# Kernel tuning notes

Hardware: AMD Instinct MI355X
Metric: run time of the kernel (lower is better)

The kernel has to match this reference:

```python
import jax, jax.numpy as jnp
import numpy as np

N = 100000   # nodes
E = 1200000  # edges
D = 64       # emb_dim
XIN = 18     # x_dim + node_dim
XD = 16      # x_dim (output)
ED = 1       # edge_dim
L = 4        # num message-passing layers
G = 8        # graphs in batch (for global_mean_pool)


def setup_inputs() -> dict:
    key = jax.random.key(0)
    ks = iter(jax.random.split(key, 64))
    def nrm(shape, s=0.05):
        return jax.random.normal(next(ks), shape, dtype=jnp.float32) * s
    inp = {}
    inp["x"] = jax.random.normal(next(ks), (N, XIN), dtype=jnp.float32)
    inp["edge_attr"] = jax.random.normal(next(ks), (E, ED), dtype=jnp.float32)
    inp["W_in"] = nrm((XIN, D)); inp["b_in"] = jnp.zeros((D,), jnp.float32)
    # per-layer stacked params (leading dim L)
    inp["msg_W1"] = nrm((L, 2 * D + ED, D)); inp["msg_b1"] = jnp.zeros((L, D), jnp.float32)
    inp["msg_g1"] = jnp.ones((L, D), jnp.float32); inp["msg_be1"] = jnp.zeros((L, D), jnp.float32)
    inp["msg_W2"] = nrm((L, D, D)); inp["msg_b2"] = jnp.zeros((L, D), jnp.float32)
    inp["msg_g2"] = jnp.ones((L, D), jnp.float32); inp["msg_be2"] = jnp.zeros((L, D), jnp.float32)
    inp["upd_W1"] = nrm((L, 2 * D, D)); inp["upd_b1"] = jnp.zeros((L, D), jnp.float32)
    inp["upd_g1"] = jnp.ones((L, D), jnp.float32); inp["upd_be1"] = jnp.zeros((L, D), jnp.float32)
    inp["upd_W2"] = nrm((L, D, D)); inp["upd_b2"] = jnp.zeros((L, D), jnp.float32)
    inp["upd_g2"] = jnp.ones((L, D), jnp.float32); inp["upd_be2"] = jnp.zeros((L, D), jnp.float32)
    inp["reward_W"] = nrm((D, D)); inp["reward_b"] = jnp.zeros((D,), jnp.float32)
    inp["rout_W"] = nrm((D, 1)); inp["rout_b"] = jnp.zeros((1,), jnp.float32)
    inp["pred_W"] = nrm((D, D)); inp["pred_b"] = jnp.zeros((D,), jnp.float32)
    inp["pout_W"] = nrm((D, XD)); inp["pout_b"] = jnp.zeros((XD,), jnp.float32)
    inp["edge_index"] = jax.random.randint(next(ks), (2, E), 0, N)
    inp["batch"] = jnp.sort(jax.random.randint(next(ks), (N,), 0, G))
    return inp


def _bn(x, g, b, eps=1e-5):
    # BatchNorm1d in training mode: batch mean + biased variance
    m = jnp.mean(x, axis=0)
    v = jnp.mean((x - m) ** 2, axis=0)
    return (x - m) * jax.lax.rsqrt(v + eps) * g + b


def _mlp(x, W1, b1, g1, be1, W2, b2, g2, be2):
    h = jax.nn.relu(_bn(x @ W1 + b1, g1, be1))
    return jax.nn.relu(_bn(h @ W2 + b2, g2, be2))


def _forward(x, edge_attr, W_in, b_in,
             msg_W1, msg_b1, msg_g1, msg_be1, msg_W2, msg_b2, msg_g2, msg_be2,
             upd_W1, upd_b1, upd_g1, upd_be1, upd_W2, upd_b2, upd_g2, upd_be2,
             reward_W, reward_b, rout_W, rout_b, pred_W, pred_b, pout_W, pout_b,
             edge_index, batch):
    src = edge_index[0]  # j (source)
    dst = edge_index[1]  # i (target); PyG default flow source_to_target
    n = x.shape[0]
    h = x @ W_in + b_in
    for l in range(L):
        # message: gather + concat + MLP(psi)
        m = jnp.concatenate([h[dst], h[src], edge_attr], axis=-1)  # (E, 2D+ED)
        m = _mlp(m, msg_W1[l], msg_b1[l], msg_g1[l], msg_be1[l],
                 msg_W2[l], msg_b2[l], msg_g2[l], msg_be2[l])
        # aggregate: scatter-add to target nodes
        agg = jax.ops.segment_sum(m, dst, num_segments=n)  # (N, D)
        # update: concat + MLP(phi); residual add from outer network
        u = jnp.concatenate([h, agg], axis=-1)
        h = h + _mlp(u, upd_W1[l], upd_b1[l], upd_g1[l], upd_be1[l],
                     upd_W2[l], upd_b2[l], upd_g2[l], upd_be2[l])
    # reward head (computed in the original forward but not returned)
    h_reward = h @ reward_W + reward_b
    cnt = jax.ops.segment_sum(jnp.ones((n,), h.dtype), batch, num_segments=G)
    h_graph = jax.ops.segment_sum(h_reward, batch, num_segments=G) / jnp.maximum(cnt, 1.0)[:, None]
    _out_reward = h_graph @ rout_W + rout_b  # unused, matches original return
    # prediction head
    x_out = jax.nn.relu(h @ pred_W + pred_b) @ pout_W + pout_b  # (N, XD)
    return x_out


def reference(x, edge_attr, W_in, b_in,
              msg_W1, msg_b1, msg_g1, msg_be1, msg_W2, msg_b2, msg_g2, msg_be2,
              upd_W1, upd_b1, upd_g1, upd_be1, upd_W2, upd_b2, upd_g2, upd_be2,
              reward_W, reward_b, rout_W, rout_b, pred_W, pred_b, pout_W, pout_b,
              edge_index, batch):
    return _forward(x, edge_attr, W_in, b_in,
                    msg_W1, msg_b1, msg_g1, msg_be1, msg_W2, msg_b2, msg_g2, msg_be2,
                    upd_W1, upd_b1, upd_g1, upd_be1, upd_W2, upd_b2, upd_g2, upd_be2,
                    reward_W, reward_b, rout_W, rout_b, pred_W, pred_b, pout_W, pout_b,
                    edge_index, batch)
```

## Files before the change

### kernel.cpp

```cpp
#include <hip/hip_runtime.h>
#include <hip/hip_fp16.h>

typedef unsigned short u16;
typedef unsigned int u32;
typedef __attribute__((ext_vector_type(8))) unsigned short us8;
typedef __attribute__((ext_vector_type(8))) _Float16 f16x8;
typedef __attribute__((ext_vector_type(4))) float f32x4;

#define EPS 1e-5f

__device__ __forceinline__ float h2f(u16 h){ __half v; *(u16*)&v = h; return __half2float(v); }
__device__ __forceinline__ u16 f2h(float f){ __half v = __float2half(f); return *(u16*)&v; }
__device__ __forceinline__ u32 pkh(float a, float b){ return (u32)f2h(a) | ((u32)f2h(b) << 16); }

__global__ __launch_bounds__(256) void k_in(const float* __restrict__ x,
    const float* __restrict__ Win, const float* __restrict__ bin,
    float* __restrict__ h, int N){
  __shared__ float Ws[18][64];
  __shared__ float xs[64][20];
  int tid = threadIdx.x;
  for (int i = tid; i < 18*64; i += 256) Ws[i>>6][i&63] = Win[i];
  int row0 = blockIdx.x * 64;
  for (int i = tid; i < 64*18; i += 256){
    int r = i/18, k = i - r*18;
    int row = row0 + r;
    xs[r][k] = (row < N) ? x[(size_t)row*18 + k] : 0.f;
  }
  __syncthreads();
  int rq = tid >> 4, dq = tid & 15;
  float4 b4 = *(const float4*)(bin + dq*4);
  float acc[4][4];
  #pragma unroll
  for (int j=0;j<4;j++){ acc[j][0]=b4.x; acc[j][1]=b4.y; acc[j][2]=b4.z; acc[j][3]=b4.w; }
  for (int k=0;k<18;k++){
    float4 wv = *(const float4*)&Ws[k][dq*4];
    #pragma unroll
    for (int j=0;j<4;j++){
      float v = xs[rq*4+j][k];
      acc[j][0]+=v*wv.x; acc[j][1]+=v*wv.y; acc[j][2]+=v*wv.z; acc[j][3]+=v*wv.w;
    }
  }
  #pragma unroll
  for (int j=0;j<4;j++){
    int row = row0 + rq*4 + j;
    if (row < N)
      *(float4*)(h + (size_t)row*64 + dq*4) = make_float4(acc[j][0],acc[j][1],acc[j][2],acc[j][3]);
  }
}

__global__ __launch_bounds__(256) void k_pq(const float* __restrict__ h,
    const float* __restrict__ A, const float* __restrict__ B,
    u16* __restrict__ P, u16* __restrict__ Q, int N){
  __shared__ float hs[64][68];
  __shared__ float As[64][64];
  __shared__ float Bs[64][64];
  int tid = threadIdx.x;
  for (int i = tid; i < 4096; i += 256){ As[i>>6][i&63] = A[i]; Bs[i>>6][i&63] = B[i]; }
  int row0 = blockIdx.x*64;
  for (int i = tid; i < 4096; i += 256){
    int r = i>>6, k = i&63; int row = row0+r;
    hs[r][k] = (row<N)? h[(size_t)row*64+k] : 0.f;
  }
  __syncthreads();
  int rq = tid>>4, dq = tid&15;
  float ap[4][4]={}, aq[4][4]={};
  for (int k=0;k<64;k+=4){
    float4 hv[4];
    #pragma unroll
    for (int j=0;j<4;j++) hv[j] = *(const float4*)&hs[rq*4+j][k];
    #pragma unroll
    for (int kk=0;kk<4;kk++){
      float4 av = *(const float4*)&As[k+kk][dq*4];
      float4 bv = *(const float4*)&Bs[k+kk][dq*4];
      #pragma unroll
      for (int j=0;j<4;j++){
        float v = ((const float*)&hv[j])[kk];
        ap[j][0]+=v*av.x; ap[j][1]+=v*av.y; ap[j][2]+=v*av.z; ap[j][3]+=v*av.w;
        aq[j][0]+=v*bv.x; aq[j][1]+=v*bv.y; aq[j][2]+=v*bv.z; aq[j][3]+=v*bv.w;
      }
    }
  }
  #pragma unroll
  for (int j=0;j<4;j++){
    int row = row0 + rq*4 + j;
    if (row<N){
      ushort4 pk, qk;
      pk.x=f2h(ap[j][0]); pk.y=f2h(ap[j][1]); pk.z=f2h(ap[j][2]); pk.w=f2h(ap[j][3]);
      qk.x=f2h(aq[j][0]); qk.y=f2h(aq[j][1]); qk.z=f2h(aq[j][2]); qk.w=f2h(aq[j][3]);
      *(ushort4*)(P+(size_t)row*64+dq*4) = pk;
      *(ushort4*)(Q+(size_t)row*64+dq*4) = qk;
    }
  }
}

__global__ __launch_bounds__(256) void k_hist(const int* __restrict__ ei, int* __restrict__ cnt, int E){
  int e = blockIdx.x*256 + threadIdx.x;
  if (e < E) atomicAdd(&cnt[ei[E+e]], 1);
}

__global__ __launch_bounds__(256) void k_scan_a(const int* __restrict__ cnt, int* __restrict__ rp,
    int* __restrict__ bsum, int N){
  __shared__ int sm[256];
  int tid = threadIdx.x;
  int i0 = blockIdx.x*1024 + tid*4;
  int v0 = (i0+0<N)? cnt[i0+0]:0;
  int v1 = (i0+1<N)? cnt[i0+1]:0;
  int v2 = (i0+2<N)? cnt[i0+2]:0;
  int v3 = (i0+3<N)? cnt[i0+3]:0;
  int s = v0+v1+v2+v3;
  sm[tid] = s; __syncthreads();
  for (int ofs=1; ofs<256; ofs<<=1){
    int v = sm[tid];
    if (tid >= ofs) v += sm[tid-ofs];
    __syncthreads(); sm[tid] = v; __syncthreads();
  }
  int base = sm[tid] - s;
  int a0 = base+v0, a1 = a0+v1, a2 = a1+v2, a3 = a2+v3;
  if (i0+0<N) rp[i0+0]=a0;
  if (i0+1<N) rp[i0+1]=a1;
  if (i0+2<N) rp[i0+2]=a2;
  if (i0+3<N) rp[i0+3]=a3;
  if (tid==255) bsum[blockIdx.x] = sm[255];
}

__global__ void k_scan_b(int* __restrict__ bsum, int NB){
  if (threadIdx.x==0){
    int run = 0;
    for (int b=0;b<NB;b++){ int t = bsum[b]; bsum[b] = run; run += t; }
  }
}

__global__ __launch_bounds__(256) void k_scan_c(const int* __restrict__ cnt, int* __restrict__ rp,
    int* __restrict__ wr, const int* __restrict__ bsum, int N, int E){
  int tid = threadIdx.x;
  int i0 = blockIdx.x*1024 + tid*4;
  int off = bsum[blockIdx.x];
  #pragma unroll
  for (int j=0;j<4;j++){
    int i = i0+j;
    if (i<N){ int ex = off + rp[i] - cnt[i]; rp[i] = ex; wr[i] = ex; }
  }
  if (blockIdx.x==0 && tid==0) rp[N] = E;
}

__global__ __launch_bounds__(256) void k_perm(const int* __restrict__ ei, const float* __restrict__ ea,
    int* __restrict__ wr, int2* __restrict__ seS, int E){
  int e = blockIdx.x*256 + threadIdx.x;
  if (e < E){
    int dn = ei[E+e];
    int pos = atomicAdd(&wr[dn], 1);
    seS[pos] = make_int2(ei[e], __float_as_int(ea[e]));
  }
}

__global__ __launch_bounds__(256) void k_t1s(const u16* __restrict__ P, const u16* __restrict__ Q,
    const int2* __restrict__ seS, const int* __restrict__ rp,
    const float* __restrict__ c1, const float* __restrict__ b1,
    u16* __restrict__ t, float* __restrict__ stats, int N){
  int tid = threadIdx.x;
  int lane = tid & 63, w = tid >> 6;
  int sub = lane >> 5;
  int dl = (lane & 31) * 2;
  float cv0 = c1[dl], cv1 = c1[dl+1];
  float bv0 = b1[dl], bv1 = b1[dl+1];
  float s0 = 0.f, s1 = 0.f, qs0 = 0.f, qs1 = 0.f;
  for (int n = blockIdx.x*4 + w; n < N; n += gridDim.x*4){
    int a = rp[n], b = rp[n+1];
    u32 pp = *(const u32*)(P + (size_t)n*64 + dl);
    float p0 = h2f((u16)(pp & 0xffffu)) + bv0;
    float p1 = h2f((u16)(pp >> 16)) + bv1;
    int p = a + sub;
    for (; p + 2 < b; p += 4){
      int2 seA = seS[p];
      int2 seB = seS[p+2];
      u32 qA = *(const u32*)(Q + (size_t)seA.x*64 + dl);
      u32 qB = *(const u32*)(Q + (size_t)seB.x*64 + dl);
      float eaA = __int_as_float(seA.y), eaB = __int_as_float(seB.y);
      float tA0 = p0 + h2f((u16)(qA & 0xffffu)) + eaA*cv0;
      float tA1 = p1 + h2f((u16)(qA >> 16)) + eaA*cv1;
      float tB0 = p0 + h2f((u16)(qB & 0xffffu)) + eaB*cv0;
      float tB1 = p1 + h2f((u16)(qB >> 16)) + eaB*cv1;
      *(u32*)(t + (size_t)p*64 + dl) = (u32)f2h(tA0) | ((u32)f2h(tA1) << 16);
      *(u32*)(t + (size_t)(p+2)*64 + dl) = (u32)f2h(tB0) | ((u32)f2h(tB1) << 16);
      s0 += tA0 + tB0; s1 += tA1 + tB1;
      qs0 += tA0*tA0 + tB0*tB0; qs1 += tA1*tA1 + tB1*tB1;
    }
    for (; p < b; p += 2){
      int2 se = seS[p];
      u32 qq = *(const u32*)(Q + (size_t)se.x*64 + dl);
      float ea = __int_as_float(se.y);
      float t0 = p0 + h2f((u16)(qq & 0xffffu)) + ea*cv0;
      float t1 = p1 + h2f((u16)(qq >> 16)) + ea*cv1;
      *(u32*)(t + (size_t)p*64 + dl) = (u32)f2h(t0) | ((u32)f2h(t1) << 16);
      s0 += t0; s1 += t1; qs0 += t0*t0; qs1 += t1*t1;
    }
  }
  __shared__ float sS[8][64], qS[8][64];
  int idx = w*2 + sub;
  sS[idx][dl] = s0; sS[idx][dl+1] = s1;
  qS[idx][dl] = qs0; qS[idx][dl+1] = qs1;
  __syncthreads();
  if (tid < 64){
    float ts = 0.f, tq = 0.f;
    #pragma unroll
    for (int r=0;r<8;r++){ ts += sS[r][tid]; tq += qS[r][tid]; }
    atomicAdd(&stats[tid], ts);
    atomicAdd(&stats[64+tid], tq);
  }
}

__global__ __launch_bounds__(256) void k_m2s(u16* __restrict__ t,
    const float* __restrict__ g1, const float* __restrict__ be1, const float* __restrict__ stats1,
    const float* __restrict__ W2, const float* __restrict__ b2,
    float* __restrict__ stats2, int E, float invE){
  __shared__ _Float16 yL[128][72];
  __shared__ _Float16 wL[64][72];
  __shared__ float scS[64], shS[64], b2S[64];
  int tid = threadIdx.x;
  if (tid < 64){
    float m = stats1[tid]*invE;
    float v = stats1[64+tid]*invE - m*m;
    float sc = g1[tid]*rsqrtf(v + EPS);
    scS[tid] = sc; shS[tid] = be1[tid] - m*sc;
    b2S[tid] = b2[tid];
  }
  for (int i = tid; i < 4096; i += 256){
    int k = i >> 6, n = i & 63;
    wL[n][k] = (_Float16)W2[i];
  }
  __syncthreads();
  int lane = tid & 63, wv = tid >> 6;
  int arow = lane & 15;
  int kgrp = lane >> 4;
  int srow = tid >> 1, sc0 = (tid & 1)*32;
  float ssum[4] = {}, ssq[4] = {};
  int ntiles = (E + 127) >> 7;
  for (int tile = blockIdx.x; tile < ntiles; tile += gridDim.x){
    int e0 = tile << 7;
    {
      int p = e0 + srow;
      if (p < E){
        const u16* src = t + (size_t)p*64 + sc0;
        #pragma unroll
        for (int c=0;c<4;c++){
          f16x8 a = *(const f16x8*)(src + c*8);
          f16x8 v;
          #pragma unroll
          for (int j=0;j<8;j++){
            int dd = sc0 + c*8 + j;
            v[j] = (_Float16)fmaxf((float)a[j]*scS[dd] + shS[dd], 0.f);
          }
          *(f16x8*)&yL[srow][sc0 + c*8] = v;
        }
      } else {
        f16x8 z;
        #pragma unroll
        for (int j=0;j<8;j++) z[j] = (_Float16)0.f;
        #pragma unroll
        for (int c=0;c<4;c++) *(f16x8*)&yL[srow][sc0 + c*8] = z;
      }
    }
    __syncthreads();
    f32x4 acc[2][4];
    #pragma unroll
    for (int mf=0; mf<2; mf++){
      int row = 32*wv + 16*mf + arow;
      f16x8 a0 = *(const f16x8*)&yL[row][8*kgrp];
      f16x8 a1 = *(const f16x8*)&yL[row][32 + 8*kgrp];
      #pragma unroll
      for (int c=0;c<4;c++){
        f16x8 b0 = *(const f16x8*)&wL[16*c + arow][8*kgrp];
        f16x8 b1 = *(const f16x8*)&wL[16*c + arow][32 + 8*kgrp];
        f32x4 d = {0.f,0.f,0.f,0.f};
        d = __builtin_amdgcn_mfma_f32_16x16x32_f16(a0, b0, d, 0, 0, 0);
        d = __builtin_amdgcn_mfma_f32_16x16x32_f16(a1, b1, d, 0, 0, 0);
        acc[mf][c] = d;
      }
    }
    __syncthreads();
    #pragma unroll
    for (int mf=0; mf<2; mf++){
      #pragma unroll
      for (int c=0;c<4;c++){
        int col = 16*c + arow;
        float bb = b2S[col];
        #pragma unroll
        for (int r=0;r<4;r++){
          int e = e0 + 32*wv + 16*mf + 4*kgrp + r;
          if (e < E){
            float v = acc[mf][c][r] + bb;
            t[(size_t)e*64 + col] = f2h(v);
            ssum[c] += v; ssq[c] += v*v;
          }
        }
      }
    }
  }
  __syncthreads();
  float* red = (float*)yL;
  #pragma unroll
  for (int c=0;c<4;c++) red[c*256 + tid] = ssum[c];
  __syncthreads();
  if (tid < 64){
    int cc = tid >> 4;
    float s = 0.f;
    for (int g=0; g<16; g++) s += red[cc*256 + g*16 + (tid & 15)];
    atomicAdd(&stats2[tid], s);
  }
  __syncthreads();
  #pragma unroll
  for (int c=0;c<4;c++) red[c*256 + tid] = ssq[c];
  __syncthreads();
  if (tid < 64){
    int cc = tid >> 4;
    float s = 0.f;
    for (int g=0; g<16; g++) s += red[cc*256 + g*16 + (tid & 15)];
    atomicAdd(&stats2[64+tid], s);
  }
}

__global__ __launch_bounds__(256) void k_agg(const u16* __restrict__ t2, const int* __restrict__ rp,
    const float* __restrict__ g2, const float* __restrict__ be2, const float* __restrict__ stats2,
    float* __restrict__ agg, int N, float invE){
  __shared__ float scS[64], shS[64];
  int tid = threadIdx.x;
  if (tid < 64){
    float m = stats2[tid]*invE;
    float v = stats2[64+tid]*invE - m*m;
    float sc = g2[tid]*rsqrtf(v+EPS);
    scS[tid] = sc; shS[tid] = be2[tid] - m*sc;
  }
  __syncthreads();
  int lane = tid & 63, w = tid >> 6;
  int sub = lane >> 5;
  int dl = (lane & 31) * 2;
  float sc0 = scS[dl], sc1 = scS[dl+1], sh0 = shS[dl], sh1 = shS[dl+1];
  for (int n = blockIdx.x*4 + w; n < N; n += gridDim.x*4){
    int a = rp[n], b = rp[n+1];
    float a0 = 0.f, a1 = 0.f;
    int p = a + sub;
    for (; p + 2 < b; p += 4){
      u32 vA = *(const u32*)(t2 + (size_t)p*64 + dl);
      u32 vB = *(const u32*)(t2 + (size_t)(p+2)*64 + dl);
      a0 += fmaxf(h2f((u16)(vA & 0xffffu))*sc0 + sh0, 0.f)
          + fmaxf(h2f((u16)(vB & 0xffffu))*sc0 + sh0, 0.f);
      a1 += fmaxf(h2f((u16)(vA >> 16))*sc1 + sh1, 0.f)
          + fmaxf(h2f((u16)(vB >> 16))*sc1 + sh1, 0.f);
    }
    for (; p < b; p += 2){
      u32 vA = *(const u32*)(t2 + (size_t)p*64 + dl);
      a0 += fmaxf(h2f((u16)(vA & 0xffffu))*sc0 + sh0, 0.f);
      a1 += fmaxf(h2f((u16)(vA >> 16))*sc1 + sh1, 0.f);
    }
    a0 += __shfl_xor(a0, 32);
    a1 += __shfl_xor(a1, 32);
    if (sub == 0)
      *(float2*)(agg + (size_t)n*64 + dl) = make_float2(a0, a1);
  }
}

__global__ __launch_bounds__(256) void k_s1(const u16* __restrict__ P, const u16* __restrict__ Q,
    const float* __restrict__ ea, const int* __restrict__ ei,
    const float* __restrict__ c1, const float* __restrict__ b1,
    float* __restrict__ stats, int E){
  int tid = threadIdx.x;
  int d = tid & 63, w = tid >> 6;
  float cv = c1[d], bv = b1[d];
  float s = 0.f, sq = 0.f;
  for (int e = blockIdx.x*4 + w; e < E; e += gridDim.x*4){
    int dn = ei[E+e], sn = ei[e];
    float t = h2f(P[(size_t)dn*64+d]) + h2f(Q[(size_t)sn*64+d]) + ea[e]*cv + bv;
    s += t; sq += t*t;
  }
  __shared__ float sS[4][64], qS[4][64];
  sS[w][d] = s; qS[w][d] = sq;
  __syncthreads();
  if (tid < 64){
    float ts = sS[0][tid]+sS[1][tid]+sS[2][tid]+sS[3][tid];
    float tq = qS[0][tid]+qS[1][tid]+qS[2][tid]+qS[3][tid];
    atomicAdd(&stats[tid], ts);
    atomicAdd(&stats[64+tid], tq);
  }
}

__global__ __launch_bounds__(256) void k_m2b(const u16* __restrict__ P, const u16* __restrict__ Q,
    const float* __restrict__ ea, const int* __restrict__ ei,
    const float* __restrict__ c1, const float* __restrict__ b1,
    const float* __restrict__ g1, const float* __restrict__ be1,
    const float* __restrict__ stats1,
    const float* __restrict__ W2, const float* __restrict__ b2,
    float* __restrict__ stats2, int E, float invE){
  __shared__ float ys[64][68];
  __shared__ float Ws[64][64];
  __shared__ float scS[64], c1S[64], bS[64], b2S[64];
  int tid = threadIdx.x;
  if (tid < 64){
    float m = stats1[tid]*invE;
    float v = stats1[64+tid]*invE - m*m;
    float sc = g1[tid]*rsqrtf(v + EPS);
    float sh = be1[tid] - m*sc;
    scS[tid] = sc;
    c1S[tid] = c1[tid]*sc;
    bS[tid]  = b1[tid]*sc + sh;
    b2S[tid] = b2[tid];
  }
  for (int i=tid;i<4096;i+=256) Ws[i>>6][i&63] = W2[i];
  __syncthreads();
  int rq = tid>>4, dq = tid&15;
  float ssum[4]={}, ssq[4]={};
  int ntiles = (E+63)>>6;
  for (int tile = blockIdx.x; tile < ntiles; tile += gridDim.x){
    int e0 = tile<<6;
    for (int i = tid; i < 4096; i += 256){
      int el = i>>6, dd = i&63;
      int e = e0 + el;
      float y = 0.f;
      if (e < E){
        int dn = ei[E+e], sn = ei[e];
        float t = (h2f(P[(size_t)dn*64+dd]) + h2f(Q[(size_t)sn*64+dd]))*scS[dd] + ea[e]*c1S[dd] + bS[dd];
        y = fmaxf(t, 0.f);
      }
      ys[el][dd] = y;
    }
    __syncthreads();
    float acc[4][4];
    float4 b4 = *(const float4*)&b2S[dq*4];
    #pragma unroll
    for (int j=0;j<4;j++){ acc[j][0]=b4.x; acc[j][1]=b4.y; acc[j][2]=b4.z; acc[j][3]=b4.w; }
    for (int k=0;k<64;k+=4){
      float4 hv[4];
      #pragma unroll
      for (int j=0;j<4;j++) hv[j] = *(const float4*)&ys[rq*4+j][k];
      #pragma unroll
      for (int kk=0;kk<4;kk++){
        float4 wv = *(const float4*)&Ws[k+kk][dq*4];
        #pragma unroll
        for (int j=0;j<4;j++){
          float v = ((const float*)&hv[j])[kk];
          acc[j][0]+=v*wv.x; acc[j][1]+=v*wv.y; acc[j][2]+=v*wv.z; acc[j][3]+=v*wv.w;
        }
      }
    }
    #pragma unroll
    for (int j=0;j<4;j++){
      int e = e0 + rq*4 + j;
      if (e < E){
        #pragma unroll
        for (int c=0;c<4;c++){ float v=acc[j][c]; ssum[c]+=v; ssq[c]+=v*v; }
      }
    }
    __syncthreads();
  }
  float* red = &ys[0][0];
  #pragma unroll
  for (int c=0;c<4;c++) red[rq*64 + dq*4 + c] = ssum[c];
  __syncthreads();
  if (tid < 64){
    float t=0.f;
    for (int r=0;r<16;r++) t += red[r*64+tid];
    atomicAdd(&stats2[tid], t);
  }
  __syncthreads();
  #pragma unroll
  for (int c=0;c<4;c++) red[rq*64 + dq*4 + c] = ssq[c];
  __syncthreads();
  if (tid < 64){
    float t=0.f;
    for (int r=0;r<16;r++) t += red[r*64+tid];
    atomicAdd(&stats2[64+tid], t);
  }
}

__global__ __launch_bounds__(256) void k_sc_rec(const u16* __restrict__ P, const u16* __restrict__ Q,
    const float* __restrict__ ea, const int* __restrict__ ei,
    const float* __restrict__ c1, const float* __restrict__ b1,
    const float* __restrict__ g1, const float* __restrict__ be1, const float* __restrict__ stats1,
    const float* __restrict__ W2, const float* __restrict__ b2,
    const float* __restrict__ g2, const float* __restrict__ be2, const float* __restrict__ stats2,
    float* __restrict__ agg, int E, float invE){
  __shared__ float ys[64][68];
  __shared__ float Ws[64][64];
  __shared__ float scS[64], c1S[64], bS[64];
  __shared__ float s2S[64], h2S[64], b2S[64];
  int tid = threadIdx.x;
  if (tid < 64){
    float m = stats1[tid]*invE;
    float v = stats1[64+tid]*invE - m*m;
    float sc = g1[tid]*rsqrtf(v + EPS);
    scS[tid] = sc;
    c1S[tid] = c1[tid]*sc;
    bS[tid]  = b1[tid]*sc + be1[tid] - m*sc;
    float m2 = stats2[tid]*invE;
    float v2 = stats2[64+tid]*invE - m2*m2;
    float sc2 = g2[tid]*rsqrtf(v2+EPS);
    s2S[tid] = sc2; h2S[tid] = be2[tid] - m2*sc2;
    b2S[tid] = b2[tid];
  }
  for (int i=tid;i<4096;i+=256) Ws[i>>6][i&63] = W2[i];
  __syncthreads();
  int rq = tid>>4, dq = tid&15;
  int ntiles = (E+63)>>6;
  for (int tile = blockIdx.x; tile < ntiles; tile += gridDim.x){
    int e0 = tile<<6;
    for (int i = tid; i < 4096; i += 256){
      int el = i>>6, dd = i&63;
      int e = e0 + el;
      float y = 0.f;
      if (e < E){
        int dn = ei[E+e], sn = ei[e];
        float t = (h2f(P[(size_t)dn*64+dd]) + h2f(Q[(size_t)sn*64+dd]))*scS[dd] + ea[e]*c1S[dd] + bS[dd];
        y = fmaxf(t, 0.f);
      }
      ys[el][dd] = y;
    }
    __syncthreads();
    float acc[4][4];
    float4 b4 = *(const float4*)&b2S[dq*4];
    #pragma unroll
    for (int j=0;j<4;j++){ acc[j][0]=b4.x; acc[j][1]=b4.y; acc[j][2]=b4.z; acc[j][3]=b4.w; }
    for (int k=0;k<64;k+=4){
      float4 hv[4];
      #pragma unroll
      for (int j=0;j<4;j++) hv[j] = *(const float4*)&ys[rq*4+j][k];
      #pragma unroll
      for (int kk=0;kk<4;kk++){
        float4 wv = *(const float4*)&Ws[k+kk][dq*4];
        #pragma unroll
        for (int j=0;j<4;j++){
          float v = ((const float*)&hv[j])[kk];
          acc[j][0]+=v*wv.x; acc[j][1]+=v*wv.y; acc[j][2]+=v*wv.z; acc[j][3]+=v*wv.w;
        }
      }
    }
    float4 sc4 = *(const float4*)&s2S[dq*4];
    float4 sh4 = *(const float4*)&h2S[dq*4];
    #pragma unroll
    for (int j=0;j<4;j++){
      int e = e0 + rq*4 + j;
      if (e < E){
        int dn = ei[E+e];
        float y0 = fmaxf(acc[j][0]*sc4.x + sh4.x, 0.f);
        float y1 = fmaxf(acc[j][1]*sc4.y + sh4.y, 0.f);
        float y2 = fmaxf(acc[j][2]*sc4.z + sh4.z, 0.f);
        float y3 = fmaxf(acc[j][3]*sc4.w + sh4.w, 0.f);
        atomicAdd(&agg[(size_t)dn*64 + dq*4    ], y0);
        atomicAdd(&agg[(size_t)dn*64 + dq*4 + 1], y1);
        atomicAdd(&agg[(size_t)dn*64 + dq*4 + 2], y2);
        atomicAdd(&agg[(size_t)dn*64 + dq*4 + 3], y3);
      }
    }
    __syncthreads();
  }
}

__global__ __launch_bounds__(256) void k_up1(const float* __restrict__ h, const float* __restrict__ agg,
    const float* __restrict__ U1, const float* __restrict__ b1u,
    float* __restrict__ tn, float* __restrict__ stats3, int N){
  __shared__ _Float16 yL[64][136];
  __shared__ _Float16 wL[64][136];
  __shared__ float bS[64];
  int tid = threadIdx.x;
  if (tid < 64) bS[tid] = b1u[tid];
  for (int i = tid; i < 8192; i += 256){
    int k = i >> 6, n = i & 63;
    wL[n][k] = (_Float16)U1[i];
  }
  int row0 = blockIdx.x * 64;
  int srow = tid >> 2, sc0 = (tid & 3) * 16;
  {
    int row = row0 + srow;
    if (row < N){
      #pragma unroll
      for (int c=0;c<4;c++){
        float4 v = *(const float4*)(h + (size_t)row*64 + sc0 + 4*c);
        *(u32*)&yL[srow][sc0+4*c]   = pkh(v.x, v.y);
        *(u32*)&yL[srow][sc0+4*c+2] = pkh(v.z, v.w);
      }
      #pragma unroll
      for (int c=0;c<4;c++){
        float4 v = *(const float4*)(agg + (size_t)row*64 + sc0 + 4*c);
        *(u32*)&yL[srow][64+sc0+4*c]   = pkh(v.x, v.y);
        *(u32*)&yL[srow][64+sc0+4*c+2] = pkh(v.z, v.w);
      }
    } else {
      #pragma unroll
      for (int c=0;c<4;c++){
        *(u32*)&yL[srow][sc0+4*c] = 0u; *(u32*)&yL[srow][sc0+4*c+2] = 0u;
        *(u32*)&yL[srow][64+sc0+4*c] = 0u; *(u32*)&yL[srow][64+sc0+4*c+2] = 0u;
      }
    }
  }
  __syncthreads();
  int lane = tid & 63, wv = tid >> 6;
  int arow = lane & 15, kgrp = lane >> 4;
  f16x8 a[4];
  #pragma unroll
  for (int kk=0;kk<4;kk++) a[kk] = *(const f16x8*)&yL[16*wv + arow][32*kk + 8*kgrp];
  float ssum[4]={}, ssq[4]={};
  #pragma unroll
  for (int c=0;c<4;c++){
    f32x4 d = {0.f,0.f,0.f,0.f};
    #pragma unroll
    for (int kk=0;kk<4;kk++){
      f16x8 b = *(const f16x8*)&wL[16*c + arow][32*kk + 8*kgrp];
      d = __builtin_amdgcn_mfma_f32_16x16x32_f16(a[kk], b, d, 0, 0, 0);
    }
    int col = 16*c + arow;
    float bb = bS[col];
    #pragma unroll
    for (int r=0;r<4;r++){
      int row = row0 + 16*wv + 4*kgrp + r;
      if (row < N){
        float v = d[r] + bb;
        tn[(size_t)row*64 + col] = v;
        ssum[c]+=v; ssq[c]+=v*v;
      }
    }
  }
  __syncthreads();
  float* red = (float*)yL;
  #pragma unroll
  for (int c=0;c<4;c++) red[c*256 + tid] = ssum[c];
  __syncthreads();
  if (tid < 64){
    int cc = tid >> 4;
    float s = 0.f;
    for (int g=0; g<16; g++) s += red[cc*256 + g*16 + (tid & 15)];
    atomicAdd(&stats3[tid], s);
  }
  __syncthreads();
  #pragma unroll
  for (int c=0;c<4;c++) red[c*256 + tid] = ssq[c];
  __syncthreads();
  if (tid < 64){
    int cc = tid >> 4;
    float s = 0.f;
    for (int g=0; g<16; g++) s += red[cc*256 + g*16 + (tid & 15)];
    atomicAdd(&stats3[64+tid], s);
  }
}

__global__ __launch_bounds__(256) void k_up2(float* __restrict__ tn,
    const float* __restrict__ g3, const float* __restrict__ be3, const float* __restrict__ stats3,
    const float* __restrict__ U2, const float* __restrict__ b2u,
    float* __restrict__ stats4, int N, float invN){
  __shared__ _Float16 yL[64][72];
  __shared__ _Float16 wL[64][72];
  __shared__ float scS[64], shS[64], bS[64];
  int tid = threadIdx.x;
  if (tid < 64){
    float m = stats3[tid]*invN;
    float v = stats3[64+tid]*invN - m*m;
    float sc = g3[tid]*rsqrtf(v+EPS);
    scS[tid] = sc; shS[tid] = be3[tid] - m*sc; bS[tid] = b2u[tid];
  }
  for (int i = tid; i < 4096; i += 256){
    int k = i >> 6, n = i & 63;
    wL[n][k] = (_Float16)U2[i];
  }
  __syncthreads();
  int row0 = blockIdx.x * 64;
  int srow = tid >> 2, sc0 = (tid & 3) * 16;
  {
    int row = row0 + srow;
    if (row < N){
      #pragma unroll
      for (int c=0;c<4;c++){
        float4 v = *(const float4*)(tn + (size_t)row*64 + sc0 + 4*c);
        int d0 = sc0 + 4*c;
        float y0 = fmaxf(v.x*scS[d0  ] + shS[d0  ], 0.f);
        float y1 = fmaxf(v.y*scS[d0+1] + shS[d0+1], 0.f);
        float y2 = fmaxf(v.z*scS[d0+2] + shS[d0+2], 0.f);
        float y3 = fmaxf(v.w*scS[d0+3] + shS[d0+3], 0.f);
        *(u32*)&yL[srow][d0]   = pkh(y0, y1);
        *(u32*)&yL[srow][d0+2] = pkh(y2, y3);
      }
    } else {
      #pragma unroll
      for (int c=0;c<4;c++){
        *(u32*)&yL[srow][sc0+4*c] = 0u; *(u32*)&yL[srow][sc0+4*c+2] = 0u;
      }
    }
  }
  __syncthreads();
  int lane = tid & 63, wv = tid >> 6;
  int arow = lane & 15, kgrp = lane >> 4;
  f16x8 a0 = *(const f16x8*)&yL[16*wv + arow][8*kgrp];
  f16x8 a1 = *(const f16x8*)&yL[16*wv + arow][32 + 8*kgrp];
  float ssum[4]={}, ssq[4]={};
  #pragma unroll
  for (int c=0;c<4;c++){
    f16x8 b0 = *(const f16x8*)&wL[16*c + arow][8*kgrp];
    f16x8 b1 = *(const f16x8*)&wL[16*c + arow][32 + 8*kgrp];
    f32x4 d = {0.f,0.f,0.f,0.f};
    d = __builtin_amdgcn_mfma_f32_16x16x32_f16(a0, b0, d, 0, 0, 0);
    d = __builtin_amdgcn_mfma_f32_16x16x32_f16(a1, b1, d, 0, 0, 0);
    int col = 16*c + arow;
    float bb = bS[col];
    #pragma unroll
    for (int r=0;r<4;r++){
      int row = row0 + 16*wv + 4*kgrp + r;
      if (row < N){
        float v = d[r] + bb;
        tn[(size_t)row*64 + col] = v;
        ssum[c]+=v; ssq[c]+=v*v;
      }
    }
  }
  __syncthreads();
  float* red = (float*)yL;
  #pragma unroll
  for (int c=0;c<4;c++) red[c*256 + tid] = ssum[c];
  __syncthreads();
  if (tid < 64){
    int cc = tid >> 4;
    float s = 0.f;
    for (int g=0; g<16; g++) s += red[cc*256 + g*16 + (tid & 15)];
    atomicAdd(&stats4[tid], s);
  }
  __syncthreads();
  #pragma unroll
  for (int c=0;c<4;c++) red[c*256 + tid] = ssq[c];
  __syncthreads();
  if (tid < 64){
    int cc = tid >> 4;
    float s = 0.f;
    for (int g=0; g<16; g++) s += red[cc*256 + g*16 + (tid & 15)];
    atomicAdd(&stats4[64+tid], s);
  }
}

__global__ __launch_bounds__(256) void k_res_pq(float* __restrict__ h, const float* __restrict__ tn,
    const float* __restrict__ g4, const float* __restrict__ be4, const float* __restrict__ stats4,
    const float* __restrict__ A, const float* __restrict__ B,
    u16* __restrict__ P, u16* __restrict__ Q, int N, float invN){
  __shared__ _Float16 yL[64][72];
  __shared__ _Float16 wLa[64][72];
  __shared__ _Float16 wLb[64][72];
  __shared__ float scS[64], shS[64];
  int tid = threadIdx.x;
  if (tid < 64){
    float m = stats4[tid]*invN;
    float v = stats4[64+tid]*invN - m*m;
    float sc = g4[tid]*rsqrtf(v+EPS);
    scS[tid] = sc; shS[tid] = be4[tid] - m*sc;
  }
  for (int i = tid; i < 4096; i += 256){
    int k = i >> 6, n = i & 63;
    wLa[n][k] = (_Float16)A[i];
    wLb[n][k] = (_Float16)B[i];
  }
  __syncthreads();
  int row0 = blockIdx.x * 64;
  int srow = tid >> 2, sc0 = (tid & 3) * 16;
  {
    int row = row0 + srow;
    if (row < N){
      #pragma unroll
      for (int c=0;c<4;c++){
        int d0 = sc0 + 4*c;
        float4 hv4 = *(const float4*)(h + (size_t)row*64 + d0);
        float4 tv4 = *(const float4*)(tn + (size_t)row*64 + d0);
        float h0 = hv4.x + fmaxf(tv4.x*scS[d0  ] + shS[d0  ], 0.f);
        float h1 = hv4.y + fmaxf(tv4.y*scS[d0+1] + shS[d0+1], 0.f);
        float h2 = hv4.z + fmaxf(tv4.z*scS[d0+2] + shS[d0+2], 0.f);
        float h3 = hv4.w + fmaxf(tv4.w*scS[d0+3] + shS[d0+3], 0.f);
        *(float4*)(h + (size_t)row*64 + d0) = make_float4(h0,h1,h2,h3);
        *(u32*)&yL[srow][d0]   = pkh(h0, h1);
        *(u32*)&yL[srow][d0+2] = pkh(h2, h3);
      }
    } else {
      #pragma unroll
      for (int c=0;c<4;c++){
        *(u32*)&yL[srow][sc0+4*c] = 0u; *(u32*)&yL[srow][sc0+4*c+2] = 0u;
      }
    }
  }
  __syncthreads();
  int lane = tid & 63, wv = tid >> 6;
  int arow = lane & 15, kgrp = lane >> 4;
  f16x8 y0 = *(const f16x8*)&yL[16*wv + arow][8*kgrp];
  f16x8 y1 = *(const f16x8*)&yL[16*wv + arow][32 + 8*kgrp];
  int node = row0 + 16*wv + arow;
  #pragma unroll
  for (int c=0;c<4;c++){
    f16x8 wa0 = *(const f16x8*)&wLa[16*c + arow][8*kgrp];
    f16x8 wa1 = *(const f16x8*)&wLa[16*c + arow][32 + 8*kgrp];
    f32x4 dp = {0.f,0.f,0.f,0.f};
    dp = __builtin_amdgcn_mfma_f32_16x16x32_f16(wa0, y0, dp, 0, 0, 0);
    dp = __builtin_amdgcn_mfma_f32_16x16x32_f16(wa1, y1, dp, 0, 0, 0);
    f16x8 wb0 = *(const f16x8*)&wLb[16*c + arow][8*kgrp];
    f16x8 wb1 = *(const f16x8*)&wLb[16*c + arow][32 + 8*kgrp];
    f32x4 dq = {0.f,0.f,0.f,0.f};
    dq = __builtin_amdgcn_mfma_f32_16x16x32_f16(wb0, y0, dq, 0, 0, 0);
    dq = __builtin_amdgcn_mfma_f32_16x16x32_f16(wb1, y1, dq, 0, 0, 0);
    if (node < N){
      ushort4 pk4, qk4;
      pk4.x = f2h(dp[0]); pk4.y = f2h(dp[1]); pk4.z = f2h(dp[2]); pk4.w = f2h(dp[3]);
      qk4.x = f2h(dq[0]); qk4.y = f2h(dq[1]); qk4.z = f2h(dq[2]); qk4.w = f2h(dq[3]);
      *(ushort4*)(P + (size_t)node*64 + 16*c + 4*kgrp) = pk4;
      *(ushort4*)(Q + (size_t)node*64 + 16*c + 4*kgrp) = qk4;
    }
  }
}

__global__ __launch_bounds__(256) void k_res_head(const float* __restrict__ h, const float* __restrict__ tn,
    const float* __restrict__ g4, const float* __restrict__ be4, const float* __restrict__ stats4,
    const float* __restrict__ Wp, const float* __restrict__ bp,
    const float* __restrict__ Wo, const float* __restrict__ bo,
    float* __restrict__ out, int N, float invN){
  __shared__ float hs[64][68];
  __shared__ float Wps[64][64];
  __shared__ float ps[64][68];
  __shared__ float Wos[64][16];
  __shared__ float scS[64], shS[64];
  int tid = threadIdx.x;
  if (tid < 64){
    float m = stats4[tid]*invN;
    float v = stats4[64+tid]*invN - m*m;
    float sc = g4[tid]*rsqrtf(v+EPS);
    scS[tid] = sc; shS[tid] = be4[tid] - m*sc;
  }
  for (int i=tid;i<4096;i+=256) Wps[i>>6][i&63] = Wp[i];
  for (int i=tid;i<1024;i+=256) Wos[i>>4][i&15] = Wo[i];
  int row0 = blockIdx.x*64;
  __syncthreads();
  for (int i = tid; i < 4096; i += 256){
    int r = i>>6, k = i&63; int row = row0+r;
    float hv = 0.f;
    if (row<N)
      hv = h[(size_t)row*64+k] + fmaxf(tn[(size_t)row*64+k]*scS[k] + shS[k], 0.f);
    hs[r][k] = hv;
  }
  __syncthreads();
  int rq = tid>>4, dq = tid&15;
  float4 b4 = *(const float4*)(bp + dq*4);
  float acc[4][4];
  #pragma unroll
  for (int j=0;j<4;j++){ acc[j][0]=b4.x; acc[j][1]=b4.y; acc[j][2]=b4.z; acc[j][3]=b4.w; }
  for (int k=0;k<64;k+=4){
    float4 hv[4];
    #pragma unroll
    for (int j=0;j<4;j++) hv[j] = *(const float4*)&hs[rq*4+j][k];
    #pragma unroll
    for (int kk=0;kk<4;kk++){
      float4 wv = *(const float4*)&Wps[k+kk][dq*4];
      #pragma unroll
      for (int j=0;j<4;j++){
        float v = ((const float*)&hv[j])[kk];
        acc[j][0]+=v*wv.x; acc[j][1]+=v*wv.y; acc[j][2]+=v*wv.z; acc[j][3]+=v*wv.w;
      }
    }
  }
  #pragma unroll
  for (int j=0;j<4;j++){
    *(float4*)&ps[rq*4+j][dq*4] = make_float4(fmaxf(acc[j][0],0.f), fmaxf(acc[j][1],0.f),
                                              fmaxf(acc[j][2],0.f), fmaxf(acc[j][3],0.f));
  }
  __syncthreads();
  int f = tid & 15;
  float bof = bo[f];
  float acc2[4] = {bof, bof, bof, bof};
  for (int k=0;k<64;k++){
    float wv = Wos[k][f];
    #pragma unroll
    for (int j=0;j<4;j++) acc2[j] += ps[rq*4+j][k]*wv;
  }
  #pragma unroll
  for (int j=0;j<4;j++){
    int row = row0 + rq*4 + j;
    if (row<N) out[(size_t)row*16 + f] = acc2[j];
  }
}

extern "C" void kernel_launch(void* const* d_in, const int* in_sizes, int n_in,
                              void* d_out, int out_size, void* d_ws, size_t ws_size,
                              hipStream_t stream){
  const float* x    = (const float*)d_in[0];
  const float* eatt = (const float*)d_in[1];
  const float* Win  = (const float*)d_in[2];
  const float* bin  = (const float*)d_in[3];
  const float* mW1  = (const float*)d_in[4];
  const float* mb1  = (const float*)d_in[5];
  const float* mg1  = (const float*)d_in[6];
  const float* mbe1 = (const float*)d_in[7];
  const float* mW2  = (const float*)d_in[8];
  const float* mb2  = (const float*)d_in[9];
  const float* mg2  = (const float*)d_in[10];
  const float* mbe2 = (const float*)d_in[11];
  const float* uW1  = (const float*)d_in[12];
  const float* ub1  = (const float*)d_in[13];
  const float* ug1  = (const float*)d_in[14];
  const float* ube1 = (const float*)d_in[15];
  const float* uW2  = (const float*)d_in[16];
  const float* ub2  = (const float*)d_in[17];
  const float* ug2  = (const float*)d_in[18];
  const float* ube2 = (const float*)d_in[19];
  const float* predW = (const float*)d_in[24];
  const float* predb = (const float*)d_in[25];
  const float* poutW = (const float*)d_in[26];
  const float* poutb = (const float*)d_in[27];
  const int*   ei    = (const int*)d_in[28];

  const int N = in_sizes[0] / 18;
  const int E = in_sizes[1];

  size_t nodeB = (size_t)N * 64 * sizeof(float);
  size_t halfB = (size_t)N * 64 * sizeof(u16);
  size_t t2B   = (size_t)E * 64 * sizeof(u16);
  size_t statsB = 16 * 128 * sizeof(float);
  int NB = (N + 1023)/1024;
  size_t csrB = (size_t)E*8 + (size_t)(N+1)*4 + (size_t)N*4 + (size_t)N*4 + 4096*4;

  bool planA = ws_size >= nodeB + 2*halfB + nodeB + t2B + csrB + statsB;

  char* w = (char*)d_ws;
  float* h = (float*)w; w += nodeB;
  u16* P = (u16*)w; w += halfB;
  u16* Q = (u16*)w; w += halfB;
  float* agg = (float*)w; w += nodeB;
  float* tn = agg;
  u16*  t2 = nullptr;
  int2* seS = nullptr;
  int *rp=nullptr, *cnt=nullptr, *wrp=nullptr, *bsum=nullptr;
  float* stats;
  if (planA){
    t2   = (u16*)w;  w += t2B;
    seS  = (int2*)w; w += (size_t)E*8;
    rp   = (int*)w;  w += (size_t)(N+1)*4;
    cnt  = (int*)w;  w += (size_t)N*4;
    wrp  = (int*)w;  w += (size_t)N*4;
    bsum = (int*)w;  w += 4096*4;
    stats = (float*)w;
  } else {
    stats = (float*)w;
  }

  hipMemsetAsync(stats, 0, statsB, stream);

  int nb = (N + 63)/64;
  float invE = 1.0f/(float)E, invN = 1.0f/(float)N;

  k_in<<<nb, 256, 0, stream>>>(x, Win, bin, h, N);
  k_pq<<<nb, 256, 0, stream>>>(h, mW1, mW1 + 4096, P, Q, N);

  if (planA){
    hipMemsetAsync(cnt, 0, (size_t)N*4, stream);
    k_hist<<<(E+255)/256, 256, 0, stream>>>(ei, cnt, E);
    k_scan_a<<<NB, 256, 0, stream>>>(cnt, rp, bsum, N);
    k_scan_b<<<1, 64, 0, stream>>>(bsum, NB);
    k_scan_c<<<NB, 256, 0, stream>>>(cnt, rp, wrp, bsum, N, E);
    k_perm<<<(E+255)/256, 256, 0, stream>>>(ei, eatt, wrp, seS, E);
  }

  for (int l = 0; l < 4; ++l){
    float* s1 = stats + (l*4+0)*128;
    float* s2 = stats + (l*4+1)*128;
    float* s3 = stats + (l*4+2)*128;
    float* s4 = stats + (l*4+3)*128;
    const float* A  = mW1 + (size_t)l*8256;
    const float* c1 = A + 8192;
    if (planA){
      k_t1s<<<2048, 256, 0, stream>>>(P, Q, seS, rp, c1, mb1 + l*64, t2, s1, N);
      k_m2s<<<2048, 256, 0, stream>>>(t2, mg1 + l*64, mbe1 + l*64, s1,
                                      mW2 + (size_t)l*4096, mb2 + l*64, s2, E, invE);
      k_agg<<<2048, 256, 0, stream>>>(t2, rp, mg2 + l*64, mbe2 + l*64, s2, agg, N, invE);
    } else {
      k_s1<<<2048, 256, 0, stream>>>(P, Q, eatt, ei, c1, mb1 + l*64, s1, E);
      k_m2b<<<1024, 256, 0, stream>>>(P, Q, eatt, ei, c1, mb1 + l*64, mg1 + l*64, mbe1 + l*64,
                                      s1, mW2 + (size_t)l*4096, mb2 + l*64, s2, E, invE);
      hipMemsetAsync(agg, 0, nodeB, stream);
      k_sc_rec<<<1024, 256, 0, stream>>>(P, Q, eatt, ei, c1, mb1 + l*64, mg1 + l*64, mbe1 + l*64,
                                         s1, mW2 + (size_t)l*4096, mb2 + l*64,
                                         mg2 + l*64, mbe2 + l*64, s2, agg, E, invE);
    }
    k_up1<<<nb, 256, 0, stream>>>(h, agg, uW1 + (size_t)l*8192, ub1 + l*64, tn, s3, N);
    k_up2<<<nb, 256, 0, stream>>>(tn, ug1 + l*64, ube1 + l*64, s3, uW2 + (size_t)l*4096,
                                  ub2 + l*64, s4, N, invN);
    if (l < 3){
      const float* An = mW1 + (size_t)(l+1)*8256;
      k_res_pq<<<nb, 256, 0, stream>>>(h, tn, ug2 + l*64, ube2 + l*64, s4,
                                       An, An + 4096, P, Q, N, invN);
    } else {
      k_res_head<<<nb, 256, 0, stream>>>(h, tn, ug2 + l*64, ube2 + l*64, s4,
                                         predW, predb, poutW, poutb, (float*)d_out, N, invN);
    }
  }
}
```

Before: 1.929 ms.

## Prefetch next edge tile into registers and store MFMA output as vectorized rows

In the second message-MLP GEMM kernel, the next tile's fp16 input rows are prefetched into registers while the current tile is normalized and multiplied. The MFMA operands are swapped so each lane holds four consecutive output columns of one edge, which allows 8-byte vectorized stores instead of scattered 2-byte stores. The per-lane statistics accumulators grow to 16 values per lane, and the final block reduction is reorganized to match. This raises register pressure and makes the reduction loop longer.

```diff
diff --git a/kernel.cpp b/kernel.cpp
--- a/kernel.cpp
+++ b/kernel.cpp
@@ -233,88 +233,119 @@
   int arow = lane & 15;
   int kgrp = lane >> 4;
   int srow = tid >> 1, sc0 = (tid & 1)*32;
-  float ssum[4] = {}, ssq[4] = {};
+  float bb[4][4];
+  #pragma unroll
+  for (int c=0;c<4;c++){
+    #pragma unroll
+    for (int r=0;r<4;r++) bb[c][r] = b2S[16*c + 4*kgrp + r];
+  }
+  float ssum[4][4] = {}, ssq[4][4] = {};
   int ntiles = (E + 127) >> 7;
+  f16x8 ra, rb, rc, rd;
+  {
+    f16x8 z;
+    #pragma unroll
+    for (int j=0;j<8;j++) z[j] = (_Float16)0.f;
+    ra = rb = rc = rd = z;
+    int tile = blockIdx.x;
+    int p = tile*128 + srow;
+    if (tile < ntiles && p < E){
+      const u16* src = t + (size_t)p*64 + sc0;
+      ra = *(const f16x8*)(src);
+      rb = *(const f16x8*)(src + 8);
+      rc = *(const f16x8*)(src + 16);
+      rd = *(const f16x8*)(src + 24);
+    }
+  }
   for (int tile = blockIdx.x; tile < ntiles; tile += gridDim.x){
     int e0 = tile << 7;
     {
-      int p = e0 + srow;
-      if (p < E){
-        const u16* src = t + (size_t)p*64 + sc0;
-        #pragma unroll
-        for (int c=0;c<4;c++){
-          f16x8 a = *(const f16x8*)(src + c*8);
-          f16x8 v;
+      f16x8 v;
+      #pragma unroll
+      for (int j=0;j<8;j++){ int dd = sc0 + j;      v[j] = (_Float16)fmaxf((float)ra[j]*scS[dd] + shS[dd], 0.f); }
+      *(f16x8*)&yL[srow][sc0]      = v;
+      #pragma unroll
+      for (int j=0;j<8;j++){ int dd = sc0 + 8 + j;  v[j] = (_Float16)fmaxf((float)rb[j]*scS[dd] + shS[dd], 0.f); }
+      *(f16x8*)&yL[srow][sc0 + 8]  = v;
+      #pragma unroll
+      for (int j=0;j<8;j++){ int dd = sc0 + 16 + j; v[j] = (_Float16)fmaxf((float)rc[j]*scS[dd] + shS[dd], 0.f); }
+      *(f16x8*)&yL[srow][sc0 + 16] = v;
+      #pragma unroll
+      for (int j=0;j<8;j++){ int dd = sc0 + 24 + j; v[j] = (_Float16)fmaxf((float)rd[j]*scS[dd] + shS[dd], 0.f); }
+      *(f16x8*)&yL[srow][sc0 + 24] = v;
+    }
+    {
+      int nt = tile + gridDim.x;
+      if (nt < ntiles){
+        int p = nt*128 + srow;
+        if (p < E){
+          const u16* src = t + (size_t)p*64 + sc0;
+          ra = *(const f16x8*)(src);
+          rb = *(const f16x8*)(src + 8);
+          rc = *(const f16x8*)(src + 16);
+          rd = *(const f16x8*)(src + 24);
+        } else {
+          f16x8 z;
           #pragma unroll
-          for (int j=0;j<8;j++){
-            int dd = sc0 + c*8 + j;
-            v[j] = (_Float16)fmaxf((float)a[j]*scS[dd] + shS[dd], 0.f);
-          }
-          *(f16x8*)&yL[srow][sc0 + c*8] = v;
+          for (int j=0;j<8;j++) z[j] = (_Float16)0.f;
+          ra = rb = rc = rd = z;
         }
-      } else {
-        f16x8 z;
-        #pragma unroll
-        for (int j=0;j<8;j++) z[j] = (_Float16)0.f;
-        #pragma unroll
-        for (int c=0;c<4;c++) *(f16x8*)&yL[srow][sc0 + c*8] = z;
       }
     }
     __syncthreads();
-    f32x4 acc[2][4];
     #pragma unroll
     for (int mf=0; mf<2; mf++){
       int row = 32*wv + 16*mf + arow;
-      f16x8 a0 = *(const f16x8*)&yL[row][8*kgrp];
-      f16x8 a1 = *(const f16x8*)&yL[row][32 + 8*kgrp];
+      f16x8 y0 = *(const f16x8*)&yL[row][8*kgrp];
+      f16x8 y1 = *(const f16x8*)&yL[row][32 + 8*kgrp];
+      int e = e0 + 32*wv + 16*mf + arow;
       #pragma unroll
       for (int c=0;c<4;c++){
-        f16x8 b0 = *(const f16x8*)&wL[16*c + arow][8*kgrp];
-        f16x8 b1 = *(const f16x8*)&wL[16*c + arow][32 + 8*kgrp];
+        f16x8 w0 = *(const f16x8*)&wL[16*c + arow][8*kgrp];
+        f16x8 w1 = *(const f16x8*)&wL[16*c + arow][32 + 8*kgrp];
         f32x4 d = {0.f,0.f,0.f,0.f};
-        d = __builtin_amdgcn_mfma_f32_16x16x32_f16(a0, b0, d, 0, 0, 0);
-        d = __builtin_amdgcn_mfma_f32_16x16x32_f16(a1, b1, d, 0, 0, 0);
-        acc[mf][c] = d;
+        d = __builtin_amdgcn_mfma_f32_16x16x32_f16(w0, y0, d, 0, 0, 0);
+        d = __builtin_amdgcn_mfma_f32_16x16x32_f16(w1, y1, d, 0, 0, 0);
+        if (e < E){
+          float v0 = d[0] + bb[c][0];
+          float v1 = d[1] + bb[c][1];
+          float v2 = d[2] + bb[c][2];
+          float v3 = d[3] + bb[c][3];
+          ushort4 st;
+          st.x = f2h(v0); st.y = f2h(v1); st.z = f2h(v2); st.w = f2h(v3);
+          *(ushort4*)(t + (size_t)e*64 + 16*c + 4*kgrp) = st;
+          ssum[c][0]+=v0; ssum[c][1]+=v1; ssum[c][2]+=v2; ssum[c][3]+=v3;
+          ssq[c][0]+=v0*v0; ssq[c][1]+=v1*v1; ssq[c][2]+=v2*v2; ssq[c][3]+=v3*v3;
+        }
       }
     }
     __syncthreads();
-    #pragma unroll
-    for (int mf=0; mf<2; mf++){
-      #pragma unroll
-      for (int c=0;c<4;c++){
-        int col = 16*c + arow;
-        float bb = b2S[col];
-        #pragma unroll
-        for (int r=0;r<4;r++){
-          int e = e0 + 32*wv + 16*mf + 4*kgrp + r;
-          if (e < E){
-            float v = acc[mf][c][r] + bb;
-            t[(size_t)e*64 + col] = f2h(v);
-            ssum[c] += v; ssq[c] += v*v;
-          }
-        }
-      }
-    }
-  }
-  __syncthreads();
+  }
   float* red = (float*)yL;
-  #pragma unroll
-  for (int c=0;c<4;c++) red[c*256 + tid] = ssum[c];
-  __syncthreads();
-  if (tid < 64){
-    int cc = tid >> 4;
+  int slot = wv*16 + arow;
+  #pragma unroll
+  for (int c=0;c<4;c++){
+    #pragma unroll
+    for (int r=0;r<4;r++)
+      red[(16*c + 4*kgrp + r)*64 + slot] = ssum[c][r];
+  }
+  __syncthreads();
+  if (tid < 64){
     float s = 0.f;
-    for (int g=0; g<16; g++) s += red[cc*256 + g*16 + (tid & 15)];
+    for (int g=0; g<64; g++) s += red[tid*64 + g];
     atomicAdd(&stats2[tid], s);
   }
   __syncthreads();
   #pragma unroll
-  for (int c=0;c<4;c++) red[c*256 + tid] = ssq[c];
-  __syncthreads();
-  if (tid < 64){
-    int cc = tid >> 4;
+  for (int c=0;c<4;c++){
+    #pragma unroll
+    for (int r=0;r<4;r++)
+      red[(16*c + 4*kgrp + r)*64 + slot] = ssq[c][r];
+  }
+  __syncthreads();
+  if (tid < 64){
     float s = 0.f;
-    for (int g=0; g<16; g++) s += red[cc*256 + g*16 + (tid & 15)];
+    for (int g=0; g<64; g++) s += red[tid*64 + g];
     atomicAdd(&stats2[64+tid], s);
   }
 }
```

New measurement: 1.854 ms. 3.9% less time.
